# Kernel tuning notes

Measured on AMD Instinct MI355X. Metric: run time of the kernel, lower is better.

Reference implementation:

```python
import jax, jax.numpy as jnp
import numpy as np

N_IN = 16384
G = 64            # input grid resolution
K_UP = 8          # 2^3 children per voxel for kernel=2 stride=2 generative transpose conv
N_OUT = N_IN * K_UP
G2 = 2 * G        # output grid resolution
NUMS = 32768      # top-k prune budget
C = 64


def _np_coords_and_maps():
    """Build voxel coords, the 27-offset kernel map on upsampled coords, and a fake GT mask."""
    rng = np.random.default_rng(0)
    flat = rng.choice(G ** 3, size=N_IN, replace=False)
    c = np.stack(np.unravel_index(flat, (G, G, G)), axis=1).astype(np.int64)  # [N_IN,3]
    offs2 = np.stack(np.meshgrid(*([[0, 1]] * 3), indexing='ij'), -1).reshape(-1, 3)  # [8,3]
    cu = (2 * c[:, None, :] + offs2[None]).reshape(-1, 3)  # [N_OUT,3], order n*8+k
    lut = np.full(G2 ** 3, N_OUT, dtype=np.int64)
    key = (cu[:, 0] * G2 + cu[:, 1]) * G2 + cu[:, 2]
    lut[key] = np.arange(N_OUT)
    offs3 = np.stack(np.meshgrid(*([[-1, 0, 1]] * 3), indexing='ij'), -1).reshape(-1, 3)  # [27,3]
    nbr = np.empty((27, N_OUT), np.int64)
    for k, d in enumerate(offs3):
        q = cu + d
        valid = ((q >= 0) & (q < G2)).all(1)
        qk = np.where(valid, (q[:, 0] * G2 + q[:, 1]) * G2 + q[:, 2], 0)
        nbr[k] = np.where(valid, lut[qk], N_OUT)  # N_OUT = sentinel 'missing'
    gt = rng.random(N_OUT) < 0.3  # isin(out.C, ground_truth.C) membership mask
    return nbr.astype(np.int32), gt


def setup_inputs() -> dict:
    key = jax.random.key(0)
    ks = jax.random.split(key, 10)
    nbr, gt = _np_coords_and_maps()
    s = 0.05
    rn = lambda k, shape: jax.random.normal(k, shape, jnp.float32) * s
    z = lambda shape: jnp.zeros(shape, jnp.float32)
    return {
        "x_feats": jax.random.normal(ks[0], (N_IN, C), jnp.float32),
        "Wup": rn(ks[1], (K_UP, C, C)), "bup": z((C,)),
        "Wc0": rn(ks[2], (27, C, C)), "bc0": z((C,)),
        "W00": rn(ks[3], (3, 27, C, C // 4)), "b00": z((3, C // 4)),
        "W01": rn(ks[4], (3, 27, C // 4, C // 2)), "b01": z((3, C // 2)),
        "W10": rn(ks[5], (3, C, C // 4)), "b10": z((3, C // 4)),
        "W11": rn(ks[6], (3, 27, C // 4, C // 4)), "b11": z((3, C // 4)),
        "W12": rn(ks[7], (3, C // 4, C // 2)), "b12": z((3, C // 2)),
        "Wcls": rn(ks[8], (27, C, 1)), "bcls": z((1,)),
        "nbr_idx": jnp.asarray(nbr), "mask_true": jnp.asarray(gt),
        "nums": NUMS,
    }


def sparse_conv(feats, nbr, W, b):
    """Gather-GEMM-scatter sparse conv: feats [N,Cin], nbr [K,N] (N = missing), W [K,Cin,Cout]."""
    fp = jnp.concatenate([feats, jnp.zeros((1, feats.shape[1]), feats.dtype)], axis=0)
    def body(acc, wn):
        Wk, nk = wn
        return acc + fp[nk] @ Wk, None
    acc0 = jnp.zeros((feats.shape[0], W.shape[-1]), feats.dtype)
    out, _ = jax.lax.scan(body, acc0, (W, nbr))
    return out + b


def reference(x_feats, Wup, bup, Wc0, bc0, W00, b00, W01, b01, W10, b10, W11, b11, W12, b12, Wcls, bcls, nbr_idx, mask_true, nums):
    # generative transpose conv k=2 s=2: each voxel emits 8 children (no overlaps)
    up = jnp.einsum('nc,kcd->nkd', x_feats, Wup).reshape(-1, Wup.shape[-1]) + bup  # [N_OUT,C]
    out = jax.nn.relu(up)
    out = jax.nn.relu(sparse_conv(out, nbr_idx, Wc0, bc0))
    for i in range(3):  # 3 InceptionResNet blocks
        o0 = sparse_conv(jax.nn.relu(sparse_conv(out, nbr_idx, W00[i], b00[i])), nbr_idx, W01[i], b01[i])
        t = jax.nn.relu(out @ W10[i] + b10[i])            # 1x1 conv
        t = jax.nn.relu(sparse_conv(t, nbr_idx, W11[i], b11[i]))
        o1 = t @ W12[i] + b12[i]                          # 1x1 conv
        out = jnp.concatenate([o0, o1], axis=1) + out
    out_cls = sparse_conv(out, nbr_idx, Wcls, bcls)       # [N_OUT,1]
    _, idx = jax.lax.top_k(out_cls[:, 0], nums)           # istopk
    mask = jnp.zeros((out.shape[0],), bool).at[idx].set(True) | mask_true  # topk + isin(GT)
    pruned = out * mask[:, None].astype(out.dtype)        # pruning as mask (static shape)
    return out_cls, pruned, mask
```

## Files before the change

kernel.cpp:

```cpp
#include <hip/hip_runtime.h>
#include <cstdint>

#define NOUTC 131072
#define NINC  16384

using uint = unsigned int;

__device__ __forceinline__ uint fkey(float v){
  uint u = __float_as_uint(v);
  return (u & 0x80000000u) ? ~u : (u | 0x80000000u);
}

template<int ROWS, int CIN, int COUT, int SPLIT, int THREADS, int NK,
         bool IDENT, bool RELU, bool RESID>
__global__ __launch_bounds__(THREADS)
void spconv2(const float* __restrict__ feats, const int* __restrict__ nbr,
             const float* __restrict__ Wg, const float* __restrict__ bias,
             const float* __restrict__ resid, float* __restrict__ outp,
             int ostride, int coff)
{
  constexpr int RG = ROWS / 8, CG = COUT / 8;
  static_assert(RG * CG * SPLIT == THREADS, "bad thread tiling");
  constexpr int CIPT = CIN / SPLIT;
  static_assert(CIPT * SPLIT == CIN, "");
  constexpr int STR  = ROWS + 4;
  constexpr int WSTR = COUT + 4;
  constexpr int TPR  = THREADS / ROWS;
  static_assert(TPR * ROWS == THREADS, "");
  constexpr int FSTG = CIN / TPR;
  static_assert(FSTG % 4 == 0, "");
  constexpr int WSTG = (CIN * COUT) / THREADS;
  constexpr int NSLOT = THREADS / SPLIT;

  constexpr int MAIN_FL = CIN * STR + CIN * WSTR;
  constexpr int RED_FL  = (SPLIT > 1) ? (THREADS / 2) * 64 : 0;
  constexpr int LDS_FL  = MAIN_FL > RED_FL ? MAIN_FL : RED_FL;
  __shared__ float smem[LDS_FL];
  float* ft = smem;
  float* Wl = smem + CIN * STR;

  const int t    = threadIdx.x;
  const int base = blockIdx.x * ROWS;
  const int sp   = t % SPLIT;
  const int slot = t / SPLIT;
  const int rg = slot / CG, cg = slot % CG;
  const int trr = rg * 8, tcc = cg * 8;
  const int gr = t / TPR, part = t % TPR;

  float4 fstg[FSTG / 4];
  alignas(16) float wstg[WSTG];
  float acc[8][8];
  #pragma unroll
  for (int a = 0; a < 8; ++a)
    #pragma unroll
    for (int b = 0; b < 8; ++b) acc[a][b] = 0.f;

  auto load_f = [&](int k) {
    int gidx = IDENT ? (base + gr) : nbr[(size_t)k * NOUTC + base + gr];
    const float4* src = reinterpret_cast<const float4*>(feats + (size_t)gidx * CIN + part * FSTG);
    #pragma unroll
    for (int j = 0; j < FSTG / 4; ++j) fstg[j] = src[j];
  };
  auto load_w = [&](int k) {
    const float* wsrc = Wg + (size_t)k * CIN * COUT + t * WSTG;
    if constexpr (WSTG % 4 == 0) {
      #pragma unroll
      for (int m = 0; m < WSTG / 4; ++m)
        *reinterpret_cast<float4*>(&wstg[4 * m]) = reinterpret_cast<const float4*>(wsrc)[m];
    } else {
      *reinterpret_cast<float2*>(&wstg[0]) = *reinterpret_cast<const float2*>(wsrc);
    }
  };

  load_f(0); load_w(0);

  for (int k = 0; k < NK; ++k) {
    #pragma unroll
    for (int j = 0; j < FSTG / 4; ++j) {
      int ci = part * FSTG + 4 * j;
      ft[(ci + 0) * STR + gr] = fstg[j].x;
      ft[(ci + 1) * STR + gr] = fstg[j].y;
      ft[(ci + 2) * STR + gr] = fstg[j].z;
      ft[(ci + 3) * STR + gr] = fstg[j].w;
    }
    #pragma unroll
    for (int m = 0; m < WSTG; ++m) {
      int widx = t * WSTG + m;
      Wl[(widx / COUT) * WSTR + (widx % COUT)] = wstg[m];
    }
    __syncthreads();
    if (k + 1 < NK) { load_f(k + 1); load_w(k + 1); }
    #pragma unroll 4
    for (int i = 0; i < CIPT; ++i) {
      int ci = sp + SPLIT * i;
      float4 f0 = *reinterpret_cast<const float4*>(&ft[ci * STR + trr]);
      float4 f1 = *reinterpret_cast<const float4*>(&ft[ci * STR + trr + 4]);
      float4 w0 = *reinterpret_cast<const float4*>(&Wl[ci * WSTR + tcc]);
      float4 w1 = *reinterpret_cast<const float4*>(&Wl[ci * WSTR + tcc + 4]);
      float fv[8] = {f0.x, f0.y, f0.z, f0.w, f1.x, f1.y, f1.z, f1.w};
      float wv[8] = {w0.x, w0.y, w0.z, w0.w, w1.x, w1.y, w1.z, w1.w};
      #pragma unroll
      for (int a = 0; a < 8; ++a)
        #pragma unroll
        for (int b = 0; b < 8; ++b)
          acc[a][b] = fmaf(fv[a], wv[b], acc[a][b]);
    }
    __syncthreads();
  }

  if constexpr (SPLIT > 1) {
    float* red = smem;
    for (int off = SPLIT / 2; off >= 1; off >>= 1) {
      __syncthreads();
      if (sp >= off && sp < 2 * off) {
        float* dst = red + ((size_t)((sp - off) * NSLOT + slot)) * 64;
        #pragma unroll
        for (int a = 0; a < 8; ++a) {
          float4 v0 = {acc[a][0], acc[a][1], acc[a][2], acc[a][3]};
          float4 v1 = {acc[a][4], acc[a][5], acc[a][6], acc[a][7]};
          *reinterpret_cast<float4*>(dst + a * 8)     = v0;
          *reinterpret_cast<float4*>(dst + a * 8 + 4) = v1;
        }
      }
      __syncthreads();
      if (sp < off) {
        const float* s = red + ((size_t)(sp * NSLOT + slot)) * 64;
        #pragma unroll
        for (int a = 0; a < 8; ++a) {
          float4 v0 = *reinterpret_cast<const float4*>(s + a * 8);
          float4 v1 = *reinterpret_cast<const float4*>(s + a * 8 + 4);
          acc[a][0] += v0.x; acc[a][1] += v0.y; acc[a][2] += v0.z; acc[a][3] += v0.w;
          acc[a][4] += v1.x; acc[a][5] += v1.y; acc[a][6] += v1.z; acc[a][7] += v1.w;
        }
      }
    }
  }

  if (sp == 0) {
    #pragma unroll
    for (int a = 0; a < 8; ++a) {
      int r = base + trr + a;
      float o[8];
      #pragma unroll
      for (int b = 0; b < 8; ++b) {
        float v = acc[a][b] + bias[tcc + b];
        if (RELU) v = v > 0.f ? v : 0.f;
        o[b] = v;
      }
      if (RESID) {
        const float* rs = resid + (size_t)r * 64 + coff + tcc;
        float4 r0 = *reinterpret_cast<const float4*>(rs);
        float4 r1 = *reinterpret_cast<const float4*>(rs + 4);
        o[0] += r0.x; o[1] += r0.y; o[2] += r0.z; o[3] += r0.w;
        o[4] += r1.x; o[5] += r1.y; o[6] += r1.z; o[7] += r1.w;
      }
      float* dst = outp + (size_t)r * ostride + coff + tcc;
      float4 s0 = {o[0], o[1], o[2], o[3]};
      float4 s1 = {o[4], o[5], o[6], o[7]};
      *reinterpret_cast<float4*>(dst)     = s0;
      *reinterpret_cast<float4*>(dst + 4) = s1;
    }
  }
}

__global__ __launch_bounds__(256)
void upsample_kernel(const float* __restrict__ x, const float* __restrict__ Wup,
                     const float* __restrict__ bup, float* __restrict__ outp)
{
  __shared__ float Wl[64 * 64];
  __shared__ float xt[64][68];
  const int t    = threadIdx.x;
  const int tile = blockIdx.x >> 3;
  const int k    = blockIdx.x & 7;
  const int base = tile * 64;

  #pragma unroll
  for (int i = t; i < 4096; i += 256) Wl[i] = Wup[k * 4096 + i];
  {
    const int gr = t >> 2, gp = t & 3;
    const float4* src = reinterpret_cast<const float4*>(x + (size_t)(base + gr) * 64) + gp * 4;
    #pragma unroll
    for (int j = 0; j < 4; ++j) {
      float4 v = src[j];
      int ci = (gp * 4 + j) * 4;
      xt[ci + 0][gr] = v.x; xt[ci + 1][gr] = v.y;
      xt[ci + 2][gr] = v.z; xt[ci + 3][gr] = v.w;
    }
  }
  __syncthreads();
  const int tcc = (t % 16) * 4, trr = (t / 16) * 4;
  float acc[4][4];
  #pragma unroll
  for (int a = 0; a < 4; ++a)
    #pragma unroll
    for (int b = 0; b < 4; ++b) acc[a][b] = 0.f;
  #pragma unroll
  for (int ci = 0; ci < 64; ++ci) {
    float4 f = *reinterpret_cast<const float4*>(&xt[ci][trr]);
    float4 w = *reinterpret_cast<const float4*>(&Wl[ci * 64 + tcc]);
    float fv[4] = {f.x, f.y, f.z, f.w};
    float wv[4] = {w.x, w.y, w.z, w.w};
    #pragma unroll
    for (int a = 0; a < 4; ++a)
      #pragma unroll
      for (int b = 0; b < 4; ++b) acc[a][b] = fmaf(fv[a], wv[b], acc[a][b]);
  }
  #pragma unroll
  for (int a = 0; a < 4; ++a) {
    int n = base + trr + a;
    float4 o;
    float v0 = acc[a][0] + bup[tcc + 0]; o.x = v0 > 0.f ? v0 : 0.f;
    float v1 = acc[a][1] + bup[tcc + 1]; o.y = v1 > 0.f ? v1 : 0.f;
    float v2 = acc[a][2] + bup[tcc + 2]; o.z = v2 > 0.f ? v2 : 0.f;
    float v3 = acc[a][3] + bup[tcc + 3]; o.w = v3 > 0.f ? v3 : 0.f;
    *reinterpret_cast<float4*>(outp + ((size_t)n * 8 + k) * 64 + tcc) = o;
  }
}

__global__ __launch_bounds__(256)
void cls_kernel(const float* __restrict__ feats, const int* __restrict__ nbr,
                const float* __restrict__ Wcls, const float* __restrict__ bcls,
                float* __restrict__ out_cls)
{
  const int wave = threadIdx.x >> 6;
  const int lane = threadIdx.x & 63;
  float wreg[27];
  #pragma unroll
  for (int k = 0; k < 27; ++k) wreg[k] = Wcls[k * 64 + lane];
  const int base = blockIdx.x * 32 + wave * 8;
  for (int rr = 0; rr < 8; ++rr) {
    const int n = base + rr;
    float s = 0.f;
    #pragma unroll
    for (int k = 0; k < 27; ++k) {
      int idx = nbr[(size_t)k * NOUTC + n];
      s = fmaf(feats[(size_t)idx * 64 + lane], wreg[k], s);
    }
    #pragma unroll
    for (int off = 32; off >= 1; off >>= 1) s += __shfl_xor(s, off, 64);
    if (lane == 0) out_cls[n] = s + bcls[0];
  }
}

__global__ void init_kernel(uint* hist1, uint* hist2, int* tie_cnt, int* flag,
                            float* fa, float* fb, float* t0, float* t1)
{
  int i = blockIdx.x * 256 + threadIdx.x;
  if (i < 65536) hist1[i] = 0;
  else if (i < 131072) hist2[i - 65536] = 0;
  if (i == 0) { tie_cnt[0] = 0; flag[0] = 0; }
  if (i < 64) { fa[(size_t)NOUTC * 64 + i] = 0.f; fb[(size_t)NOUTC * 64 + i] = 0.f; }
  if (i < 16) { t0[(size_t)NOUTC * 16 + i] = 0.f; t1[(size_t)NOUTC * 16 + i] = 0.f; }
}

__global__ void detect_kernel(const unsigned char* __restrict__ mt, int* flag)
{
  int i = blockIdx.x * 256 + threadIdx.x;
  int p = i * 4 + 1;
  if (p < NOUTC && mt[p] != 0) flag[0] = 1;
}

__global__ void hist1_kernel(const float* __restrict__ cls, uint* __restrict__ hist)
{
  for (int i = blockIdx.x * blockDim.x + threadIdx.x; i < NOUTC; i += gridDim.x * blockDim.x)
    atomicAdd(&hist[fkey(cls[i]) >> 16], 1u);
}

__global__ void scan1_kernel(const uint* __restrict__ hist, const int* __restrict__ nums,
                             uint* __restrict__ res)
{
  __shared__ uint chunk[256];
  const int t = threadIdx.x;
  uint s = 0;
  for (int j = 0; j < 256; ++j) s += hist[t * 256 + j];
  chunk[t] = s;
  __syncthreads();
  if (t == 0) {
    uint k = (uint)nums[0];
    uint cum = 0; int c = 255;
    for (; c > 0; --c) { if (cum + chunk[c] >= k) break; cum += chunk[c]; }
    int B = c * 256; uint cum2 = cum;
    for (int b = c * 256 + 255; b >= c * 256; --b) {
      if (cum2 + hist[b] >= k) { B = b; break; }
      cum2 += hist[b];
    }
    res[0] = (uint)B; res[1] = cum2;
  }
}

__global__ void hist2_kernel(const float* __restrict__ cls, const uint* __restrict__ res1,
                             uint* __restrict__ hist)
{
  const uint B = res1[0];
  for (int i = blockIdx.x * blockDim.x + threadIdx.x; i < NOUTC; i += gridDim.x * blockDim.x) {
    uint key = fkey(cls[i]);
    if ((key >> 16) == B) atomicAdd(&hist[key & 0xffffu], 1u);
  }
}

__global__ void scan2_kernel(const uint* __restrict__ hist, const uint* __restrict__ res1,
                             const int* __restrict__ nums, uint* __restrict__ res2)
{
  __shared__ uint chunk[256];
  const int t = threadIdx.x;
  uint s = 0;
  for (int j = 0; j < 256; ++j) s += hist[t * 256 + j];
  chunk[t] = s;
  __syncthreads();
  if (t == 0) {
    uint k = (uint)nums[0];
    uint cum = res1[1]; int c = 255;
    for (; c > 0; --c) { if (cum + chunk[c] >= k) break; cum += chunk[c]; }
    int L = c * 256; uint cum2 = cum;
    for (int b = c * 256 + 255; b >= c * 256; --b) {
      if (cum2 + hist[b] >= k) { L = b; break; }
      cum2 += hist[b];
    }
    res2[0] = (res1[0] << 16) | (uint)L;
    res2[1] = k - cum2;
  }
}

__global__ void mark_kernel(const float* __restrict__ cls, const uint* __restrict__ res2,
                            unsigned char* __restrict__ msel, int* tie_cnt, int* tie_idx)
{
  const uint T = res2[0];
  for (int i = blockIdx.x * blockDim.x + threadIdx.x; i < NOUTC; i += gridDim.x * blockDim.x) {
    uint key = fkey(cls[i]);
    msel[i] = key > T ? 1 : 0;
    if (key == T) {
      int p = atomicAdd(tie_cnt, 1);
      if (p < 4096) tie_idx[p] = i;
    }
  }
}

__global__ void tie_kernel(const uint* __restrict__ res2, const int* __restrict__ tie_cnt,
                           const int* __restrict__ tie_idx, unsigned char* __restrict__ msel)
{
  int need = (int)res2[1];
  int cnt = tie_cnt[0]; if (cnt > 4096) cnt = 4096;
  if (need <= 0) return;
  if (cnt <= need) {
    for (int i = threadIdx.x; i < cnt; i += 256) msel[tie_idx[i]] = 1;
  } else {
    for (int i = threadIdx.x; i < cnt; i += 256) {
      int my = tie_idx[i];
      int rank = 0;
      for (int j = 0; j < cnt; ++j) rank += (tie_idx[j] < my) ? 1 : 0;
      if (rank < need) msel[my] = 1;
    }
  }
}

__global__ void prune_kernel(const float* __restrict__ feats, const unsigned char* __restrict__ msel,
                             const void* __restrict__ mtrue, const int* __restrict__ flag,
                             float* __restrict__ dout)
{
  const unsigned char* mb = (const unsigned char*)mtrue;
  const int* mi = (const int*)mtrue;
  const bool bytes = (flag[0] != 0);
  float* pruned = dout + NOUTC;
  float* maskf  = dout + NOUTC + (size_t)NOUTC * 64;
  const float4* src = reinterpret_cast<const float4*>(feats);
  float4* dst = reinterpret_cast<float4*>(pruned);
  const int total = NOUTC * 16;
  for (int i = blockIdx.x * blockDim.x + threadIdx.x; i < total; i += gridDim.x * blockDim.x) {
    int n = i >> 4;
    bool mt = bytes ? (mb[n] != 0) : (mi[n] != 0);
    bool m = (msel[n] != 0) || mt;
    float4 v = src[i];
    float4 z = {0.f, 0.f, 0.f, 0.f};
    dst[i] = m ? v : z;
    if ((i & 15) == 0) maskf[n] = m ? 1.f : 0.f;
  }
}

extern "C" void kernel_launch(void* const* d_in, const int* in_sizes, int n_in,
                              void* d_out, int out_size, void* d_ws, size_t ws_size,
                              hipStream_t stream)
{
  const float* x    = (const float*)d_in[0];
  const float* Wup  = (const float*)d_in[1];
  const float* bup  = (const float*)d_in[2];
  const float* Wc0  = (const float*)d_in[3];
  const float* bc0  = (const float*)d_in[4];
  const float* W00  = (const float*)d_in[5];
  const float* b00  = (const float*)d_in[6];
  const float* W01  = (const float*)d_in[7];
  const float* b01  = (const float*)d_in[8];
  const float* W10  = (const float*)d_in[9];
  const float* b10  = (const float*)d_in[10];
  const float* W11  = (const float*)d_in[11];
  const float* b11  = (const float*)d_in[12];
  const float* W12  = (const float*)d_in[13];
  const float* b12  = (const float*)d_in[14];
  const float* Wcls = (const float*)d_in[15];
  const float* bcls = (const float*)d_in[16];
  const int*   nbr  = (const int*)d_in[17];
  const void*  mtrue= d_in[18];
  const int*   nums = (const int*)d_in[19];

  float* dout = (float*)d_out;

  float* fa = (float*)d_ws;
  float* t0 = fa + (size_t)(NOUTC + 1) * 64;
  float* t1 = t0 + (size_t)(NOUTC + 1) * 16;
  uint*  hist1 = (uint*)(t1 + (size_t)(NOUTC + 1) * 16);
  uint*  hist2 = hist1 + 65536;
  uint*  res1  = hist2 + 65536;
  uint*  res2  = res1 + 2;
  int*   tie_cnt = (int*)(res2 + 2);
  int*   flag    = tie_cnt + 1;
  int*   tie_idx = flag + 1;
  unsigned char* msel = (unsigned char*)(tie_idx + 4096);
  float* fb = dout + NOUTC;

  init_kernel<<<512, 256, 0, stream>>>(hist1, hist2, tie_cnt, flag, fa, fb, t0, t1);
  detect_kernel<<<128, 256, 0, stream>>>((const unsigned char*)mtrue, flag);

  upsample_kernel<<<2048, 256, 0, stream>>>(x, Wup, bup, fa);

  spconv2<128, 64, 64, 2, 256, 27, false, true, false>
      <<<NOUTC / 128, 256, 0, stream>>>(fa, nbr, Wc0, bc0, nullptr, fb, 64, 0);

  const float* cur = fb; float* nxt = fa;
  for (int i = 0; i < 3; ++i) {
    spconv2<128, 64, 16, 4, 128, 27, false, true, false>
        <<<NOUTC / 128, 128, 0, stream>>>(cur, nbr, W00 + (size_t)i * 27 * 64 * 16,
                                          b00 + i * 16, nullptr, t0, 16, 0);
    spconv2<128, 16, 32, 4, 256, 27, false, false, true>
        <<<NOUTC / 128, 256, 0, stream>>>(t0, nbr, W01 + (size_t)i * 27 * 16 * 32,
                                          b01 + i * 32, cur, nxt, 64, 0);
    spconv2<128, 64, 16, 4, 128, 1, true, true, false>
        <<<NOUTC / 128, 128, 0, stream>>>(cur, nullptr, W10 + (size_t)i * 64 * 16,
                                          b10 + i * 16, nullptr, t1, 16, 0);
    spconv2<128, 16, 16, 4, 128, 27, false, true, false>
        <<<NOUTC / 128, 128, 0, stream>>>(t1, nbr, W11 + (size_t)i * 27 * 16 * 16,
                                          b11 + i * 16, nullptr, t0, 16, 0);
    spconv2<128, 16, 32, 4, 256, 1, true, false, true>
        <<<NOUTC / 128, 256, 0, stream>>>(t0, nullptr, W12 + (size_t)i * 16 * 32,
                                          b12 + i * 32, cur, nxt, 64, 32);
    float* tmp = (float*)cur; cur = nxt; nxt = tmp;
  }

  cls_kernel<<<NOUTC / 32, 256, 0, stream>>>(cur, nbr, Wcls, bcls, dout);

  hist1_kernel<<<512, 256, 0, stream>>>(dout, hist1);
  scan1_kernel<<<1, 256, 0, stream>>>(hist1, nums, res1);
  hist2_kernel<<<512, 256, 0, stream>>>(dout, res1, hist2);
  scan2_kernel<<<1, 256, 0, stream>>>(hist2, res1, nums, res2);
  mark_kernel<<<512, 256, 0, stream>>>(dout, res2, msel, tie_cnt, tie_idx);
  tie_kernel<<<1, 256, 0, stream>>>(res2, tie_cnt, tie_idx, msel);
  prune_kernel<<<4096, 256, 0, stream>>>(cur, msel, mtrue, flag, dout);
}
```

Before: 1.297 ms.

## Split sparse conv into dense sibling part and compacted cross-block neighbor gathers

The 27-tap convolutions (Wc0 and W00) are split in two. Taps that land inside the same 2x2x2 upsample block are computed densely with a fixed tap lookup. The rare neighbors outside the block are compacted per tap into an entry list, multiplied per tap into a slab, and added back with bias and ReLU in a combine kernel. The classifier conv is also reordered to first compute 27 per-voxel dot products and then gather 27 scalars per row, rather than gathering full 64-channel features. This adds several kernels, compaction passes and slab traffic, and relies on a fixed capacity CAP for the out-of-block neighbors.

```diff
diff --git a/kernel.cpp b/kernel.cpp
--- a/kernel.cpp
+++ b/kernel.cpp
@@ -3,12 +3,585 @@
 
 #define NOUTC 131072
 #define NINC  16384
+#define CAP   204800
+#define NCH   128
+#define MAXB  3328
 
 using uint = unsigned int;
 
 __device__ __forceinline__ uint fkey(float v){
   uint u = __float_as_uint(v);
   return (u & 0x80000000u) ? ~u : (u | 0x80000000u);
+}
+
+__device__ __forceinline__ int ktap(int o, int q){
+  int d0 = ((q>>2)&1) - ((o>>2)&1);
+  int d1 = ((q>>1)&1) - ((o>>1)&1);
+  int d2 = (q&1) - (o&1);
+  return (d0+1)*9 + (d1+1)*3 + (d2+1);
+}
+__device__ __forceinline__ bool is_sib(int o, int k){
+  int k0 = k/9, k1 = (k%9)/3, k2 = k%3;
+  int q0 = ((o>>2)&1) + k0 - 1;
+  int q1 = ((o>>1)&1) + k1 - 1;
+  int q2 = (o&1)      + k2 - 1;
+  return (q0>=0 && q0<=1 && q1>=0 && q1<=1 && q2>=0 && q2<=1);
+}
+
+__global__ __launch_bounds__(256)
+void count_kernel(const int* __restrict__ nbr, uint* __restrict__ counts)
+{
+  int k = blockIdx.x / NCH, cb = blockIdx.x % NCH;
+  int t = threadIdx.x;
+  int cnt = 0;
+  for (int s = 0; s < 4; ++s){
+    int row = cb*1024 + s*256 + t;
+    int idx = nbr[(size_t)k*NOUTC + row];
+    bool f = (idx != NOUTC) && !is_sib(row & 7, k);
+    cnt += __syncthreads_count(f);
+  }
+  if (t == 0) counts[blockIdx.x] = (uint)cnt;
+}
+
+__global__ __launch_bounds__(256)
+void scan_kernel(const uint* __restrict__ counts, uint* __restrict__ choff,
+                 int* __restrict__ karr)
+{
+  __shared__ uint kt[27], segs[27], sege[27];
+  int t = threadIdx.x;
+  if (t < 27){ uint s = 0; for (int cb = 0; cb < NCH; ++cb) s += counts[t*NCH+cb]; kt[t] = s; }
+  __syncthreads();
+  if (t == 0){
+    uint run = 0;
+    for (int k = 0; k < 27; ++k){
+      segs[k] = run;
+      uint pad = (kt[k] + 63u) & ~63u;
+      if (run + pad > CAP) pad = (run < CAP) ? ((CAP - run) & ~63u) : 0;
+      run += pad;
+      sege[k] = run;
+    }
+  }
+  __syncthreads();
+  if (t < 27){
+    uint run = segs[t];
+    for (int cb = 0; cb < NCH; ++cb){ choff[t*NCH+cb] = run; run += counts[t*NCH+cb]; }
+  }
+  __syncthreads();
+  for (int b = t; b < MAXB; b += 256){
+    int kk = -1; uint e = (uint)b * 64u;
+    for (int k = 0; k < 27; ++k) if (e >= segs[k] && e < sege[k]) kk = k;
+    karr[b] = kk;
+  }
+}
+
+__global__ __launch_bounds__(256)
+void fill_kernel(const int* __restrict__ nbr, const uint* __restrict__ choff,
+                 uint2* __restrict__ entries)
+{
+  __shared__ uint wc[4][4];
+  __shared__ uint sbase[4];
+  int k = blockIdx.x / NCH, cb = blockIdx.x % NCH;
+  int t = threadIdx.x, w = t >> 6, l = t & 63;
+  uint base = choff[blockIdx.x];
+  int rows[4], idxs[4];
+  unsigned long long bal[4];
+  for (int s = 0; s < 4; ++s){
+    int row = cb*1024 + s*256 + t;
+    int idx = nbr[(size_t)k*NOUTC + row];
+    bool f = (idx != NOUTC) && !is_sib(row & 7, k);
+    bal[s] = __ballot(f);
+    if (l == 0) wc[s][w] = (uint)__popcll(bal[s]);
+    rows[s] = row; idxs[s] = idx;
+  }
+  __syncthreads();
+  if (t == 0){
+    uint r = 0;
+    for (int s = 0; s < 4; ++s){ sbase[s] = r; for (int w2 = 0; w2 < 4; ++w2) r += wc[s][w2]; }
+  }
+  __syncthreads();
+  for (int s = 0; s < 4; ++s){
+    if ((bal[s] >> l) & 1ull){
+      uint off = sbase[s];
+      for (int w2 = 0; w2 < w; ++w2) off += wc[s][w2];
+      off += (uint)__popcll(bal[s] & ((1ull << l) - 1ull));
+      uint pos = base + off;
+      if (pos < CAP) entries[pos] = make_uint2((uint)rows[s], (uint)idxs[s]);
+    }
+  }
+}
+
+__global__ __launch_bounds__(256)
+void c0sib_kernel(const float* __restrict__ feats, const float* __restrict__ Wc0,
+                  const float* __restrict__ bias, float* __restrict__ outp)
+{
+  __shared__ float smem[1280 + 14688];
+  float* ft = smem;
+  float* wb = smem + 1280;
+  const int t = threadIdx.x, w = t >> 6, l = t & 63;
+  const int o = l >> 3, pg = (l >> 2) & 1, cg = l & 3;
+  const int base = blockIdx.x * 128;
+
+  int kt8[8];
+  #pragma unroll
+  for (int q = 0; q < 8; ++q) kt8[q] = ktap(o, q);
+
+  float acc[8][16];
+  #pragma unroll
+  for (int a = 0; a < 8; ++a)
+    #pragma unroll
+    for (int j = 0; j < 16; ++j) acc[a][j] = 0.f;
+
+  for (int ch = 0; ch < 8; ++ch){
+    {
+      int row = base + (t >> 1), part = t & 1;
+      float4 v = *reinterpret_cast<const float4*>(feats + (size_t)row*64 + ch*8 + part*4);
+      int oo = row & 7, pp = (row >> 3) & 15;
+      int cl = part * 4;
+      ft[((cl+0)*8 + oo)*20 + pp] = v.x;
+      ft[((cl+1)*8 + oo)*20 + pp] = v.y;
+      ft[((cl+2)*8 + oo)*20 + pp] = v.z;
+      ft[((cl+3)*8 + oo)*20 + pp] = v.w;
+    }
+    for (int e = t; e < 3456; e += 256){
+      int c4 = e & 15, kk = (e >> 4) % 27, ci = (e >> 4) / 27;
+      float4 v = *reinterpret_cast<const float4*>(Wc0 + (size_t)kk*4096 + (ch*8+ci)*64 + c4*4);
+      *reinterpret_cast<float4*>(&wb[(ci*27 + kk)*68 + c4*4]) = v;
+    }
+    __syncthreads();
+    #pragma unroll
+    for (int ii = 0; ii < 2; ++ii){
+      int ci = w * 2 + ii;
+      #pragma unroll
+      for (int q = 0; q < 8; ++q){
+        const float* fp = &ft[(ci*8 + q)*20 + pg*8];
+        float4 f0 = *reinterpret_cast<const float4*>(fp);
+        float4 f1 = *reinterpret_cast<const float4*>(fp + 4);
+        float fv[8] = {f0.x,f0.y,f0.z,f0.w, f1.x,f1.y,f1.z,f1.w};
+        const float* wp = &wb[(ci*27 + kt8[q])*68 + cg*16];
+        float4 w0 = *reinterpret_cast<const float4*>(wp);
+        float4 w1 = *reinterpret_cast<const float4*>(wp + 4);
+        float4 w2 = *reinterpret_cast<const float4*>(wp + 8);
+        float4 w3 = *reinterpret_cast<const float4*>(wp + 12);
+        float wv[16] = {w0.x,w0.y,w0.z,w0.w, w1.x,w1.y,w1.z,w1.w,
+                        w2.x,w2.y,w2.z,w2.w, w3.x,w3.y,w3.z,w3.w};
+        #pragma unroll
+        for (int a = 0; a < 8; ++a)
+          #pragma unroll
+          for (int j = 0; j < 16; ++j)
+            acc[a][j] = fmaf(fv[a], wv[j], acc[a][j]);
+      }
+    }
+    __syncthreads();
+  }
+
+  float* red = wb;
+  #pragma unroll
+  for (int hh = 0; hh < 2; ++hh){
+    if (w >= 2){
+      float* d = &red[((w-2)*64 + l)*68];
+      #pragma unroll
+      for (int a = 0; a < 8; ++a){
+        float4 v0 = {acc[a][hh*8+0], acc[a][hh*8+1], acc[a][hh*8+2], acc[a][hh*8+3]};
+        float4 v1 = {acc[a][hh*8+4], acc[a][hh*8+5], acc[a][hh*8+6], acc[a][hh*8+7]};
+        *reinterpret_cast<float4*>(d + a*8)     = v0;
+        *reinterpret_cast<float4*>(d + a*8 + 4) = v1;
+      }
+    }
+    __syncthreads();
+    if (w < 2){
+      const float* s2 = &red[(w*64 + l)*68];
+      #pragma unroll
+      for (int a = 0; a < 8; ++a)
+        #pragma unroll
+        for (int j = 0; j < 8; ++j) acc[a][hh*8+j] += s2[a*8+j];
+    }
+    __syncthreads();
+    if (w == 1){
+      float* d = &red[l*68];
+      #pragma unroll
+      for (int a = 0; a < 8; ++a)
+        #pragma unroll
+        for (int j = 0; j < 8; ++j) d[a*8+j] = acc[a][hh*8+j];
+    }
+    __syncthreads();
+    if (w == 0){
+      const float* s2 = &red[l*68];
+      #pragma unroll
+      for (int a = 0; a < 8; ++a)
+        #pragma unroll
+        for (int j = 0; j < 8; ++j) acc[a][hh*8+j] += s2[a*8+j];
+    }
+    __syncthreads();
+  }
+
+  if (w == 0){
+    #pragma unroll
+    for (int pp = 0; pp < 8; ++pp){
+      int row = base + (pg*8 + pp)*8 + o;
+      float* dst = outp + (size_t)row*64 + cg*16;
+      #pragma unroll
+      for (int m = 0; m < 4; ++m){
+        float4 v = {acc[pp][m*4+0] + bias[cg*16+m*4+0],
+                    acc[pp][m*4+1] + bias[cg*16+m*4+1],
+                    acc[pp][m*4+2] + bias[cg*16+m*4+2],
+                    acc[pp][m*4+3] + bias[cg*16+m*4+3]};
+        *reinterpret_cast<float4*>(dst + m*4) = v;
+      }
+    }
+  }
+}
+
+__global__ __launch_bounds__(256)
+void asib_kernel(const float* __restrict__ feats, const float* __restrict__ W00i,
+                 const float* __restrict__ b00i, float* __restrict__ t0)
+{
+  __shared__ float smem[8704];
+  float* ft = smem;
+  float* wb = smem + 2304;
+  const int t = threadIdx.x, w = t >> 6, l = t & 63;
+  const int o = l >> 3, pg = l & 7;
+  const int base = blockIdx.x * 256;
+
+  int kt8[8];
+  #pragma unroll
+  for (int q = 0; q < 8; ++q) kt8[q] = ktap(o, q);
+
+  float acc[4][16];
+  #pragma unroll
+  for (int a = 0; a < 4; ++a)
+    #pragma unroll
+    for (int j = 0; j < 16; ++j) acc[a][j] = 0.f;
+
+  for (int ch = 0; ch < 8; ++ch){
+    {
+      int row = base + t;
+      float4 v0 = *reinterpret_cast<const float4*>(feats + (size_t)row*64 + ch*8);
+      float4 v1 = *reinterpret_cast<const float4*>(feats + (size_t)row*64 + ch*8 + 4);
+      int oo = row & 7, pp = (row >> 3) & 31;
+      ft[((0)*8 + oo)*36 + pp] = v0.x; ft[((1)*8 + oo)*36 + pp] = v0.y;
+      ft[((2)*8 + oo)*36 + pp] = v0.z; ft[((3)*8 + oo)*36 + pp] = v0.w;
+      ft[((4)*8 + oo)*36 + pp] = v1.x; ft[((5)*8 + oo)*36 + pp] = v1.y;
+      ft[((6)*8 + oo)*36 + pp] = v1.z; ft[((7)*8 + oo)*36 + pp] = v1.w;
+    }
+    for (int e = t; e < 864; e += 256){
+      int c4 = e & 3, kk = (e >> 2) % 27, ci = (e >> 2) / 27;
+      float4 v = *reinterpret_cast<const float4*>(W00i + (size_t)kk*1024 + (ch*8+ci)*16 + c4*4);
+      *reinterpret_cast<float4*>(&wb[(ci*27 + kk)*20 + c4*4]) = v;
+    }
+    __syncthreads();
+    #pragma unroll
+    for (int ii = 0; ii < 2; ++ii){
+      int ci = w * 2 + ii;
+      #pragma unroll
+      for (int q = 0; q < 8; ++q){
+        float4 f0 = *reinterpret_cast<const float4*>(&ft[(ci*8 + q)*36 + pg*4]);
+        float fv[4] = {f0.x, f0.y, f0.z, f0.w};
+        const float* wp = &wb[(ci*27 + kt8[q])*20];
+        float4 w0 = *reinterpret_cast<const float4*>(wp);
+        float4 w1 = *reinterpret_cast<const float4*>(wp + 4);
+        float4 w2 = *reinterpret_cast<const float4*>(wp + 8);
+        float4 w3 = *reinterpret_cast<const float4*>(wp + 12);
+        float wv[16] = {w0.x,w0.y,w0.z,w0.w, w1.x,w1.y,w1.z,w1.w,
+                        w2.x,w2.y,w2.z,w2.w, w3.x,w3.y,w3.z,w3.w};
+        #pragma unroll
+        for (int a = 0; a < 4; ++a)
+          #pragma unroll
+          for (int j = 0; j < 16; ++j)
+            acc[a][j] = fmaf(fv[a], wv[j], acc[a][j]);
+      }
+    }
+    __syncthreads();
+  }
+
+  float* red = smem;
+  if (w >= 2){
+    float* d = &red[((w-2)*64 + l)*68];
+    #pragma unroll
+    for (int a = 0; a < 4; ++a){
+      #pragma unroll
+      for (int m = 0; m < 4; ++m){
+        float4 v = {acc[a][m*4+0], acc[a][m*4+1], acc[a][m*4+2], acc[a][m*4+3]};
+        *reinterpret_cast<float4*>(d + a*16 + m*4) = v;
+      }
+    }
+  }
+  __syncthreads();
+  if (w < 2){
+    const float* s2 = &red[(w*64 + l)*68];
+    #pragma unroll
+    for (int a = 0; a < 4; ++a)
+      #pragma unroll
+      for (int j = 0; j < 16; ++j) acc[a][j] += s2[a*16+j];
+  }
+  __syncthreads();
+  if (w == 1){
+    float* d = &red[l*68];
+    #pragma unroll
+    for (int a = 0; a < 4; ++a)
+      #pragma unroll
+      for (int j = 0; j < 16; ++j) d[a*16+j] = acc[a][j];
+  }
+  __syncthreads();
+  if (w == 0){
+    const float* s2 = &red[l*68];
+    #pragma unroll
+    for (int a = 0; a < 4; ++a)
+      #pragma unroll
+      for (int j = 0; j < 16; ++j) acc[a][j] += s2[a*16+j];
+    #pragma unroll
+    for (int pp = 0; pp < 4; ++pp){
+      int row = base + (pg*4 + pp)*8 + o;
+      float* dst = t0 + (size_t)row*16;
+      #pragma unroll
+      for (int m = 0; m < 4; ++m){
+        float4 v = {acc[pp][m*4+0] + b00i[m*4+0], acc[pp][m*4+1] + b00i[m*4+1],
+                    acc[pp][m*4+2] + b00i[m*4+2], acc[pp][m*4+3] + b00i[m*4+3]};
+        *reinterpret_cast<float4*>(dst + m*4) = v;
+      }
+    }
+  }
+}
+
+__global__ __launch_bounds__(128)
+void p1c0_kernel(const float* __restrict__ feats, const float* __restrict__ Wc0,
+                 const uint2* __restrict__ entries, const int* __restrict__ karr,
+                 float* __restrict__ slab, int h)
+{
+  __shared__ float ft2[64*68];
+  __shared__ float wbs[64*36];
+  int b = blockIdx.x;
+  int k = karr[b];
+  if (k < 0) return;
+  int t = threadIdx.x;
+  for (int e = t; e < 512; e += 128){
+    int ci = e >> 3, c4 = e & 7;
+    float4 v = *reinterpret_cast<const float4*>(Wc0 + (size_t)k*4096 + ci*64 + h*32 + c4*4);
+    *reinterpret_cast<float4*>(&wbs[ci*36 + c4*4]) = v;
+  }
+  {
+    int e = t >> 1, part = t & 1;
+    uint2 en = entries[(size_t)b*64 + e];
+    int gidx = (en.x == 0xFFFFFFFFu) ? NOUTC : (int)en.y;
+    const float4* src = reinterpret_cast<const float4*>(feats + (size_t)gidx*64 + part*32);
+    #pragma unroll
+    for (int j = 0; j < 8; ++j){
+      float4 v = src[j];
+      int ci = part*32 + j*4;
+      ft2[(ci+0)*68 + e] = v.x; ft2[(ci+1)*68 + e] = v.y;
+      ft2[(ci+2)*68 + e] = v.z; ft2[(ci+3)*68 + e] = v.w;
+    }
+  }
+  __syncthreads();
+  int sp = t & 1, tile = t >> 1, eg = tile >> 3, cg = tile & 7;
+  float acc[8][4];
+  #pragma unroll
+  for (int a = 0; a < 8; ++a){ acc[a][0]=0.f; acc[a][1]=0.f; acc[a][2]=0.f; acc[a][3]=0.f; }
+  for (int i = 0; i < 32; ++i){
+    int ci = sp + 2*i;
+    float4 f0 = *reinterpret_cast<const float4*>(&ft2[ci*68 + eg*8]);
+    float4 f1 = *reinterpret_cast<const float4*>(&ft2[ci*68 + eg*8 + 4]);
+    float fv[8] = {f0.x,f0.y,f0.z,f0.w, f1.x,f1.y,f1.z,f1.w};
+    float4 wv = *reinterpret_cast<const float4*>(&wbs[ci*36 + cg*4]);
+    float wa[4] = {wv.x, wv.y, wv.z, wv.w};
+    #pragma unroll
+    for (int a = 0; a < 8; ++a)
+      #pragma unroll
+      for (int j = 0; j < 4; ++j)
+        acc[a][j] = fmaf(fv[a], wa[j], acc[a][j]);
+  }
+  #pragma unroll
+  for (int a = 0; a < 8; ++a)
+    #pragma unroll
+    for (int j = 0; j < 4; ++j) acc[a][j] += __shfl_xor(acc[a][j], 1, 64);
+  if (sp == 0){
+    #pragma unroll
+    for (int a = 0; a < 8; ++a){
+      int e = eg*8 + a;
+      float4 v = {acc[a][0], acc[a][1], acc[a][2], acc[a][3]};
+      *reinterpret_cast<float4*>(&slab[((size_t)b*64 + e)*32 + cg*4]) = v;
+    }
+  }
+}
+
+__global__ __launch_bounds__(128)
+void p1a_kernel(const float* __restrict__ feats, const float* __restrict__ W00i,
+                const uint2* __restrict__ entries, const int* __restrict__ karr,
+                float* __restrict__ slab)
+{
+  __shared__ float ft2[64*68];
+  __shared__ float wbs[64*18];
+  int b = blockIdx.x;
+  int k = karr[b];
+  if (k < 0) return;
+  int t = threadIdx.x;
+  for (int e = t; e < 256; e += 128){
+    int ci = e >> 2, c4 = e & 3;
+    float4 v = *reinterpret_cast<const float4*>(W00i + (size_t)k*1024 + ci*16 + c4*4);
+    *reinterpret_cast<float4*>(&wbs[ci*18 + c4*4]) = v;
+  }
+  {
+    int e = t >> 1, part = t & 1;
+    uint2 en = entries[(size_t)b*64 + e];
+    int gidx = (en.x == 0xFFFFFFFFu) ? NOUTC : (int)en.y;
+    const float4* src = reinterpret_cast<const float4*>(feats + (size_t)gidx*64 + part*32);
+    #pragma unroll
+    for (int j = 0; j < 8; ++j){
+      float4 v = src[j];
+      int ci = part*32 + j*4;
+      ft2[(ci+0)*68 + e] = v.x; ft2[(ci+1)*68 + e] = v.y;
+      ft2[(ci+2)*68 + e] = v.z; ft2[(ci+3)*68 + e] = v.w;
+    }
+  }
+  __syncthreads();
+  int sp = t & 1, tile = t >> 1, eg = tile >> 2, cg = tile & 3;
+  float acc[4][4];
+  #pragma unroll
+  for (int a = 0; a < 4; ++a){ acc[a][0]=0.f; acc[a][1]=0.f; acc[a][2]=0.f; acc[a][3]=0.f; }
+  for (int i = 0; i < 32; ++i){
+    int ci = sp + 2*i;
+    float4 f0 = *reinterpret_cast<const float4*>(&ft2[ci*68 + eg*4]);
+    float fv[4] = {f0.x, f0.y, f0.z, f0.w};
+    float4 wv = *reinterpret_cast<const float4*>(&wbs[ci*18 + cg*4]);
+    float wa[4] = {wv.x, wv.y, wv.z, wv.w};
+    #pragma unroll
+    for (int a = 0; a < 4; ++a)
+      #pragma unroll
+      for (int j = 0; j < 4; ++j)
+        acc[a][j] = fmaf(fv[a], wa[j], acc[a][j]);
+  }
+  #pragma unroll
+  for (int a = 0; a < 4; ++a)
+    #pragma unroll
+    for (int j = 0; j < 4; ++j) acc[a][j] += __shfl_xor(acc[a][j], 1, 64);
+  if (sp == 0){
+    #pragma unroll
+    for (int a = 0; a < 4; ++a){
+      int e = eg*4 + a;
+      float4 v = {acc[a][0], acc[a][1], acc[a][2], acc[a][3]};
+      *reinterpret_cast<float4*>(&slab[((size_t)b*64 + e)*16 + cg*4]) = v;
+    }
+  }
+}
+
+__global__ __launch_bounds__(256)
+void cmbc0_kernel(const int* __restrict__ nbr, const uint* __restrict__ choff,
+                  const float* __restrict__ slab, float* __restrict__ fb, int h)
+{
+  __shared__ uint wc[4][4];
+  int cb = blockIdx.x >> 1, cq = blockIdx.x & 1;
+  int t = threadIdx.x, w = t >> 6, l = t & 63;
+  int co0 = h*32 + cq*16;
+  float acc[4][16];
+  #pragma unroll
+  for (int s = 0; s < 4; ++s)
+    #pragma unroll
+    for (int j = 0; j < 16; ++j) acc[s][j] = 0.f;
+
+  for (int k = 0; k < 27; ++k){
+    unsigned long long bal[4];
+    for (int s = 0; s < 4; ++s){
+      int row = cb*1024 + s*256 + t;
+      int idx = nbr[(size_t)k*NOUTC + row];
+      bool f = (idx != NOUTC) && !is_sib(row & 7, k);
+      bal[s] = __ballot(f);
+      if (l == 0) wc[s][w] = (uint)__popcll(bal[s]);
+    }
+    __syncthreads();
+    uint sbs[4];
+    { uint r = 0; for (int s = 0; s < 4; ++s){ sbs[s] = r; for (int w2 = 0; w2 < 4; ++w2) r += wc[s][w2]; } }
+    uint base = choff[k*NCH + cb];
+    for (int s = 0; s < 4; ++s){
+      if ((bal[s] >> l) & 1ull){
+        uint off = sbs[s];
+        for (int w2 = 0; w2 < w; ++w2) off += wc[s][w2];
+        off += (uint)__popcll(bal[s] & ((1ull << l) - 1ull));
+        uint pos = base + off;
+        if (pos < CAP){
+          const float4* sr = reinterpret_cast<const float4*>(slab + (size_t)pos*32 + cq*16);
+          float4 a0 = sr[0], a1 = sr[1], a2 = sr[2], a3 = sr[3];
+          acc[s][0]+=a0.x; acc[s][1]+=a0.y; acc[s][2]+=a0.z; acc[s][3]+=a0.w;
+          acc[s][4]+=a1.x; acc[s][5]+=a1.y; acc[s][6]+=a1.z; acc[s][7]+=a1.w;
+          acc[s][8]+=a2.x; acc[s][9]+=a2.y; acc[s][10]+=a2.z; acc[s][11]+=a2.w;
+          acc[s][12]+=a3.x; acc[s][13]+=a3.y; acc[s][14]+=a3.z; acc[s][15]+=a3.w;
+        }
+      }
+    }
+    __syncthreads();
+  }
+  for (int s = 0; s < 4; ++s){
+    int row = cb*1024 + s*256 + t;
+    float* dst = fb + (size_t)row*64 + co0;
+    #pragma unroll
+    for (int m = 0; m < 4; ++m){
+      float4 b0 = *reinterpret_cast<const float4*>(dst + m*4);
+      float4 v;
+      v.x = b0.x + acc[s][m*4+0]; v.x = v.x > 0.f ? v.x : 0.f;
+      v.y = b0.y + acc[s][m*4+1]; v.y = v.y > 0.f ? v.y : 0.f;
+      v.z = b0.z + acc[s][m*4+2]; v.z = v.z > 0.f ? v.z : 0.f;
+      v.w = b0.w + acc[s][m*4+3]; v.w = v.w > 0.f ? v.w : 0.f;
+      *reinterpret_cast<float4*>(dst + m*4) = v;
+    }
+  }
+}
+
+__global__ __launch_bounds__(256)
+void cmba_kernel(const int* __restrict__ nbr, const uint* __restrict__ choff,
+                 const float* __restrict__ slab, float* __restrict__ t0)
+{
+  __shared__ uint wc[4][4];
+  int cb = blockIdx.x;
+  int t = threadIdx.x, w = t >> 6, l = t & 63;
+  float acc[4][16];
+  #pragma unroll
+  for (int s = 0; s < 4; ++s)
+    #pragma unroll
+    for (int j = 0; j < 16; ++j) acc[s][j] = 0.f;
+
+  for (int k = 0; k < 27; ++k){
+    unsigned long long bal[4];
+    for (int s = 0; s < 4; ++s){
+      int row = cb*1024 + s*256 + t;
+      int idx = nbr[(size_t)k*NOUTC + row];
+      bool f = (idx != NOUTC) && !is_sib(row & 7, k);
+      bal[s] = __ballot(f);
+      if (l == 0) wc[s][w] = (uint)__popcll(bal[s]);
+    }
+    __syncthreads();
+    uint sbs[4];
+    { uint r = 0; for (int s = 0; s < 4; ++s){ sbs[s] = r; for (int w2 = 0; w2 < 4; ++w2) r += wc[s][w2]; } }
+    uint base = choff[k*NCH + cb];
+    for (int s = 0; s < 4; ++s){
+      if ((bal[s] >> l) & 1ull){
+        uint off = sbs[s];
+        for (int w2 = 0; w2 < w; ++w2) off += wc[s][w2];
+        off += (uint)__popcll(bal[s] & ((1ull << l) - 1ull));
+        uint pos = base + off;
+        if (pos < CAP){
+          const float4* sr = reinterpret_cast<const float4*>(slab + (size_t)pos*16);
+          float4 a0 = sr[0], a1 = sr[1], a2 = sr[2], a3 = sr[3];
+          acc[s][0]+=a0.x; acc[s][1]+=a0.y; acc[s][2]+=a0.z; acc[s][3]+=a0.w;
+          acc[s][4]+=a1.x; acc[s][5]+=a1.y; acc[s][6]+=a1.z; acc[s][7]+=a1.w;
+          acc[s][8]+=a2.x; acc[s][9]+=a2.y; acc[s][10]+=a2.z; acc[s][11]+=a2.w;
+          acc[s][12]+=a3.x; acc[s][13]+=a3.y; acc[s][14]+=a3.z; acc[s][15]+=a3.w;
+        }
+      }
+    }
+    __syncthreads();
+  }
+  for (int s = 0; s < 4; ++s){
+    int row = cb*1024 + s*256 + t;
+    float* dst = t0 + (size_t)row*16;
+    #pragma unroll
+    for (int m = 0; m < 4; ++m){
+      float4 b0 = *reinterpret_cast<const float4*>(dst + m*4);
+      float4 v;
+      v.x = b0.x + acc[s][m*4+0]; v.x = v.x > 0.f ? v.x : 0.f;
+      v.y = b0.y + acc[s][m*4+1]; v.y = v.y > 0.f ? v.y : 0.f;
+      v.z = b0.z + acc[s][m*4+2]; v.z = v.z > 0.f ? v.z : 0.f;
+      v.w = b0.w + acc[s][m*4+3]; v.w = v.w > 0.f ? v.w : 0.f;
+      *reinterpret_cast<float4*>(dst + m*4) = v;
+    }
+  }
 }
 
 template<int ROWS, int CIN, int COUT, int SPLIT, int THREADS, int NK,
@@ -22,13 +595,10 @@
   constexpr int RG = ROWS / 8, CG = COUT / 8;
   static_assert(RG * CG * SPLIT == THREADS, "bad thread tiling");
   constexpr int CIPT = CIN / SPLIT;
-  static_assert(CIPT * SPLIT == CIN, "");
   constexpr int STR  = ROWS + 4;
   constexpr int WSTR = COUT + 4;
   constexpr int TPR  = THREADS / ROWS;
-  static_assert(TPR * ROWS == THREADS, "");
   constexpr int FSTG = CIN / TPR;
-  static_assert(FSTG % 4 == 0, "");
   constexpr int WSTG = (CIN * COUT) / THREADS;
   constexpr int NSLOT = THREADS / SPLIT;
 
@@ -218,28 +788,45 @@
 }
 
 __global__ __launch_bounds__(256)
-void cls_kernel(const float* __restrict__ feats, const int* __restrict__ nbr,
-                const float* __restrict__ Wcls, const float* __restrict__ bcls,
-                float* __restrict__ out_cls)
-{
-  const int wave = threadIdx.x >> 6;
-  const int lane = threadIdx.x & 63;
-  float wreg[27];
-  #pragma unroll
-  for (int k = 0; k < 27; ++k) wreg[k] = Wcls[k * 64 + lane];
-  const int base = blockIdx.x * 32 + wave * 8;
-  for (int rr = 0; rr < 8; ++rr) {
-    const int n = base + rr;
-    float s = 0.f;
-    #pragma unroll
-    for (int k = 0; k < 27; ++k) {
-      int idx = nbr[(size_t)k * NOUTC + n];
-      s = fmaf(feats[(size_t)idx * 64 + lane], wreg[k], s);
-    }
-    #pragma unroll
-    for (int off = 32; off >= 1; off >>= 1) s += __shfl_xor(s, off, 64);
-    if (lane == 0) out_cls[n] = s + bcls[0];
-  }
+void cls1_kernel(const float* __restrict__ feats, const float* __restrict__ Wcls,
+                 float* __restrict__ g)
+{
+  const int n = blockIdx.x * 256 + threadIdx.x;
+  if (blockIdx.x == 0 && threadIdx.x < 28) g[(size_t)NOUTC * 28 + threadIdx.x] = 0.f;
+  const float4* src = reinterpret_cast<const float4*>(feats + (size_t)n * 64);
+  float f[64];
+  #pragma unroll
+  for (int j = 0; j < 16; ++j) {
+    float4 a = src[j];
+    f[4*j+0]=a.x; f[4*j+1]=a.y; f[4*j+2]=a.z; f[4*j+3]=a.w;
+  }
+  #pragma unroll 1
+  for (int k = 0; k < 27; ++k) {
+    const float* w = Wcls + k * 64;
+    float s0 = 0.f, s1 = 0.f, s2 = 0.f, s3 = 0.f;
+    #pragma unroll
+    for (int j = 0; j < 16; ++j) {
+      s0 = fmaf(f[j],      w[j],      s0);
+      s1 = fmaf(f[16 + j], w[16 + j], s1);
+      s2 = fmaf(f[32 + j], w[32 + j], s2);
+      s3 = fmaf(f[48 + j], w[48 + j], s3);
+    }
+    g[(size_t)n * 28 + k] = (s0 + s1) + (s2 + s3);
+  }
+}
+
+__global__ __launch_bounds__(256)
+void cls2_kernel(const float* __restrict__ g, const int* __restrict__ nbr,
+                 const float* __restrict__ bcls, float* __restrict__ out_cls)
+{
+  const int n = blockIdx.x * 256 + threadIdx.x;
+  float s = bcls[0];
+  #pragma unroll 1
+  for (int k = 0; k < 27; ++k) {
+    int idx = nbr[(size_t)k * NOUTC + n];
+    s += g[(size_t)idx * 28 + k];
+  }
+  out_cls[n] = s;
 }
 
 __global__ void init_kernel(uint* hist1, uint* hist2, int* tie_cnt, int* flag,
@@ -403,48 +990,65 @@
 
   float* dout = (float*)d_out;
 
-  float* fa = (float*)d_ws;
-  float* t0 = fa + (size_t)(NOUTC + 1) * 64;
-  float* t1 = t0 + (size_t)(NOUTC + 1) * 16;
-  uint*  hist1 = (uint*)(t1 + (size_t)(NOUTC + 1) * 16);
+  float* fa   = (float*)d_ws;
+  float* t0   = fa + (size_t)(NOUTC + 1) * 64;
+  float* t1   = t0 + (size_t)(NOUTC + 1) * 16;
+  float* g    = t0;
+  float* slab = t1 + (size_t)(NOUTC + 1) * 16;
+  uint*  hist1 = (uint*)(slab + (size_t)CAP * 32);
   uint*  hist2 = hist1 + 65536;
   uint*  res1  = hist2 + 65536;
   uint*  res2  = res1 + 2;
   int*   tie_cnt = (int*)(res2 + 2);
   int*   flag    = tie_cnt + 1;
   int*   tie_idx = flag + 1;
-  unsigned char* msel = (unsigned char*)(tie_idx + 4096);
+  uint*  counts  = (uint*)(tie_idx + 4096);
+  uint*  choff   = counts + 27 * NCH;
+  int*   karr    = (int*)(choff + 27 * NCH);
+  int*   meta    = karr + MAXB;
+  uint2* entries = (uint2*)(meta + 4);
+  unsigned char* msel = (unsigned char*)(entries + CAP);
   float* fb = dout + NOUTC;
 
   init_kernel<<<512, 256, 0, stream>>>(hist1, hist2, tie_cnt, flag, fa, fb, t0, t1);
   detect_kernel<<<128, 256, 0, stream>>>((const unsigned char*)mtrue, flag);
 
+  hipMemsetAsync(entries, 0xFF, (size_t)CAP * sizeof(uint2), stream);
+  count_kernel<<<27 * NCH, 256, 0, stream>>>(nbr, counts);
+  scan_kernel<<<1, 256, 0, stream>>>(counts, choff, karr);
+  fill_kernel<<<27 * NCH, 256, 0, stream>>>(nbr, choff, entries);
+
   upsample_kernel<<<2048, 256, 0, stream>>>(x, Wup, bup, fa);
 
-  spconv2<128, 64, 64, 2, 256, 27, false, true, false>
-      <<<NOUTC / 128, 256, 0, stream>>>(fa, nbr, Wc0, bc0, nullptr, fb, 64, 0);
+  c0sib_kernel<<<1024, 256, 0, stream>>>(fa, Wc0, bc0, fb);
+  p1c0_kernel<<<MAXB, 128, 0, stream>>>(fa, Wc0, entries, karr, slab, 0);
+  cmbc0_kernel<<<256, 256, 0, stream>>>(nbr, choff, slab, fb, 0);
+  p1c0_kernel<<<MAXB, 128, 0, stream>>>(fa, Wc0, entries, karr, slab, 1);
+  cmbc0_kernel<<<256, 256, 0, stream>>>(nbr, choff, slab, fb, 1);
 
   const float* cur = fb; float* nxt = fa;
   for (int i = 0; i < 3; ++i) {
-    spconv2<128, 64, 16, 4, 128, 27, false, true, false>
-        <<<NOUTC / 128, 128, 0, stream>>>(cur, nbr, W00 + (size_t)i * 27 * 64 * 16,
-                                          b00 + i * 16, nullptr, t0, 16, 0);
+    const float* W00i = W00 + (size_t)i * 27 * 1024;
+    asib_kernel<<<512, 256, 0, stream>>>(cur, W00i, b00 + i * 16, t0);
+    p1a_kernel<<<MAXB, 128, 0, stream>>>(cur, W00i, entries, karr, slab);
+    cmba_kernel<<<128, 256, 0, stream>>>(nbr, choff, slab, t0);
+    spconv2<128, 64, 16, 4, 128, 1, true, true, false>
+        <<<NOUTC / 128, 128, 0, stream>>>(cur, nullptr, W10 + (size_t)i * 1024,
+                                          b10 + i * 16, nullptr, t1, 16, 0);
     spconv2<128, 16, 32, 4, 256, 27, false, false, true>
-        <<<NOUTC / 128, 256, 0, stream>>>(t0, nbr, W01 + (size_t)i * 27 * 16 * 32,
+        <<<NOUTC / 128, 256, 0, stream>>>(t0, nbr, W01 + (size_t)i * 27 * 512,
                                           b01 + i * 32, cur, nxt, 64, 0);
-    spconv2<128, 64, 16, 4, 128, 1, true, true, false>
-        <<<NOUTC / 128, 128, 0, stream>>>(cur, nullptr, W10 + (size_t)i * 64 * 16,
-                                          b10 + i * 16, nullptr, t1, 16, 0);
     spconv2<128, 16, 16, 4, 128, 27, false, true, false>
-        <<<NOUTC / 128, 128, 0, stream>>>(t1, nbr, W11 + (size_t)i * 27 * 16 * 16,
+        <<<NOUTC / 128, 128, 0, stream>>>(t1, nbr, W11 + (size_t)i * 27 * 256,
                                           b11 + i * 16, nullptr, t0, 16, 0);
     spconv2<128, 16, 32, 4, 256, 1, true, false, true>
-        <<<NOUTC / 128, 256, 0, stream>>>(t0, nullptr, W12 + (size_t)i * 16 * 32,
+        <<<NOUTC / 128, 256, 0, stream>>>(t0, nullptr, W12 + (size_t)i * 512,
                                           b12 + i * 32, cur, nxt, 64, 32);
     float* tmp = (float*)cur; cur = nxt; nxt = tmp;
   }
 
-  cls_kernel<<<NOUTC / 32, 256, 0, stream>>>(cur, nbr, Wcls, bcls, dout);
+  cls1_kernel<<<512, 256, 0, stream>>>(cur, Wcls, g);
+  cls2_kernel<<<512, 256, 0, stream>>>(g, nbr, bcls, dout);
 
   hist1_kernel<<<512, 256, 0, stream>>>(dout, hist1);
   scan1_kernel<<<1, 256, 0, stream>>>(hist1, nums, res1);
```

Measured after the change: 1.445 ms. 1.11x slower.
